# Performance work log

Hardware: AMD Instinct MI355X
Metric: run time of the kernel (lower is better)

The kernel has to match this reference:

```python
import jax, jax.numpy as jnp
import numpy as np

DIM = 1024
NUM_HEADS = 16
WINDOW_SIZE = 512
HEAD_DIM = DIM // NUM_HEADS
SCALE = HEAD_DIM ** (-0.5)


def setup_inputs() -> dict:
    key = jax.random.key(0)
    kq, kk, kv = jax.random.split(key, 3)
    shape = (2, NUM_HEADS, 2048, HEAD_DIM)
    q = jax.random.normal(kq, shape, dtype=jnp.float32)
    k = jax.random.normal(kk, shape, dtype=jnp.float32)
    v = jax.random.normal(kv, shape, dtype=jnp.float32)
    return {"q": q, "k": k, "v": v}


def reference(q, k, v):
    B, H, N, D = q.shape
    pos = jnp.arange(N)
    # causal + sliding window: col <= row and col >= row - w + 1
    window_mask = (pos[None, :] <= pos[:, None]) & (pos[None, :] >= pos[:, None] - WINDOW_SIZE + 1)  # (N, N)
    attn = jnp.einsum("bhnd,bhmd->bhnm", q, k) * SCALE  # (B, H, N, N)
    attn = jnp.where(window_mask[None, None], attn, -jnp.inf)
    attn = jax.nn.softmax(attn, axis=-1)
    attn = jnp.nan_to_num(attn, nan=0.0)
    return jnp.einsum("bhnm,bhmd->bhnd", attn, v)
```

## Files before the change

kernel.cpp:

```cpp
#include <hip/hip_runtime.h>
#include <math.h>


#define SEQ 2048
#define HD  64
#define LDR 72

typedef short short8 __attribute__((ext_vector_type(8)));
typedef float f32x4  __attribute__((ext_vector_type(4)));

static __device__ inline unsigned short f2bf(float f){
  union{float f; unsigned u;} un; un.f=f;
  return (unsigned short)((un.u + 0x7FFFu + ((un.u>>16)&1u))>>16);
}
static __device__ inline int swz(int row){ return (row&3)|(((row>>3)&1)<<2); }

static __device__ __forceinline__ void gll16(const unsigned short* g, unsigned short* l){
  __builtin_amdgcn_global_load_lds(
    (const __attribute__((address_space(1))) unsigned int*)(const void*)g,
    (__attribute__((address_space(3))) unsigned int*)(void*)l, 16, 0, 0);
}

__global__ __launch_bounds__(256) void swa_prep(
    const float* __restrict__ k, const float* __restrict__ v,
    unsigned short* __restrict__ Kb, unsigned short* __restrict__ Vtb)
{
  __shared__ unsigned short Vs[64*68];
  const int tid=threadIdx.x, bid=blockIdx.x;
  const long tbase=(long)bid*4096;
  const float C=0.18033688011112042f;

  #pragma unroll
  for(int i=0;i<2;++i){
    int id=i*256+tid, r=id>>3, lc=id&7;
    float4 f0=*(const float4*)(k+tbase+r*64+lc*8);
    float4 f1=*(const float4*)(k+tbase+r*64+lc*8+4);
    unsigned short h[8];
    h[0]=f2bf(f0.x*C); h[1]=f2bf(f0.y*C); h[2]=f2bf(f0.z*C); h[3]=f2bf(f0.w*C);
    h[4]=f2bf(f1.x*C); h[5]=f2bf(f1.y*C); h[6]=f2bf(f1.z*C); h[7]=f2bf(f1.w*C);
    *(uint4*)(Kb+tbase+r*64+(long)((lc^swz(r))*8))=*(uint4*)h;
  }
  #pragma unroll
  for(int i=0;i<2;++i){
    int id=i*256+tid, r=id>>3, c=id&7;
    float4 f0=*(const float4*)(v+tbase+r*64+c*8);
    float4 f1=*(const float4*)(v+tbase+r*64+c*8+4);
    ushort4 a,b;
    a.x=f2bf(f0.x); a.y=f2bf(f0.y); a.z=f2bf(f0.z); a.w=f2bf(f0.w);
    b.x=f2bf(f1.x); b.y=f2bf(f1.y); b.z=f2bf(f1.z); b.w=f2bf(f1.w);
    *(ushort4*)&Vs[r*68+c*8]  =a;
    *(ushort4*)&Vs[r*68+c*8+4]=b;
  }
  __syncthreads();
  #pragma unroll
  for(int i=0;i<2;++i){
    int id=i*256+tid, d=id>>3, lc=id&7;
    unsigned short t8[8];
    #pragma unroll
    for(int e=0;e<8;++e) t8[e]=Vs[(lc*8+e)*68+d];
    *(uint4*)(Vtb+tbase+d*64+(long)((lc^swz(d))*8))=*(uint4*)t8;
  }
}

__global__ __launch_bounds__(256) void swa_main(
    const float* __restrict__ q,
    const unsigned short* __restrict__ Kb,
    const unsigned short* __restrict__ Vtb,
    float* __restrict__ out)
{
  __shared__ unsigned short Ks[2][4096];
  __shared__ unsigned short Vsh[2][4096];

  const int tid=threadIdx.x, bid=blockIdx.x;
  const int mtile=bid&31, bh=bid>>5, m0=mtile*64;
  const long base=(long)bh*SEQ*HD;
  const int wv=tid>>6, lane=tid&63, quad=lane>>4, l16=lane&15;
  const int qrow=m0+wv*16+l16;

  short8 qa[2];
  {
    const float* qp=q+base+(long)qrow*HD+quad*8;
    #pragma unroll
    for(int kk=0;kk<2;++kk){
      float4 f0=*(const float4*)(qp+kk*32);
      float4 f1=*(const float4*)(qp+kk*32+4);
      short8 a;
      a[0]=(short)f2bf(f0.x); a[1]=(short)f2bf(f0.y);
      a[2]=(short)f2bf(f0.z); a[3]=(short)f2bf(f0.w);
      a[4]=(short)f2bf(f1.x); a[5]=(short)f2bf(f1.y);
      a[6]=(short)f2bf(f1.z); a[7]=(short)f2bf(f1.w);
      qa[kk]=a;
    }
  }

  const int rbase=8*(l16>>2)+(l16&3);
  const int swk=(l16&3)|(((l16>>2)&1)<<2);
  const int swv=(l16&3)|(((l16>>3)&1)<<2);
  int kaoff[2][4], vboff[2][4];
  #pragma unroll
  for(int kk=0;kk<2;++kk){
    #pragma unroll
    for(int nt=0;nt<4;++nt)
      kaoff[kk][nt]=(rbase+(nt&1)*4+(nt>>1)*32)*64+(((quad+4*kk)^swk)*8);
    #pragma unroll
    for(int dt=0;dt<4;++dt)
      vboff[kk][dt]=(dt*16+l16)*64+(((quad+4*kk)^swv)*8);
  }

  const unsigned short* Kt=Kb +(long)bh*32*4096;
  const unsigned short* Vt=Vtb+(long)bh*32*4096;
  const int seg=wv*1024+lane*8;

  f32x4 oacc[4];
  #pragma unroll
  for(int dt=0;dt<4;++dt) oacc[dt]=(f32x4){0.f,0.f,0.f,0.f};
  float lrun=0.f;

  const int tb=mtile, tlo=(mtile>=8)?(mtile-8):0;

  gll16(Kt+(long)tlo*4096+seg,     &Ks[0][seg]);
  gll16(Kt+(long)tlo*4096+seg+512, &Ks[0][seg+512]);
  gll16(Vt+(long)tlo*4096+seg,     &Vsh[0][seg]);
  gll16(Vt+(long)tlo*4096+seg+512, &Vsh[0][seg+512]);
  __syncthreads();

#define STEP(T, BUF, MASKED) {                                                  \
    if ((T)<tb){                                                                \
      const unsigned short* kn=Kt+(long)((T)+1)*4096;                           \
      const unsigned short* vn=Vt+(long)((T)+1)*4096;                           \
      gll16(kn+seg,     &Ks[(BUF)^1][seg]);                                     \
      gll16(kn+seg+512, &Ks[(BUF)^1][seg+512]);                                 \
      gll16(vn+seg,     &Vsh[(BUF)^1][seg]);                                    \
      gll16(vn+seg+512, &Vsh[(BUF)^1][seg+512]);                                \
    }                                                                           \
    f32x4 sacc[4];                                                              \
    _Pragma("unroll") for(int nt=0;nt<4;++nt) sacc[nt]=(f32x4){0.f,0.f,0.f,0.f};\
    _Pragma("unroll") for(int kk=0;kk<2;++kk){                                  \
      _Pragma("unroll") for(int nt=0;nt<4;++nt){                                \
        short8 ka=*(const short8*)&Ks[BUF][kaoff[kk][nt]];                      \
        sacc[nt]=__builtin_amdgcn_mfma_f32_16x16x32_bf16(ka,qa[kk],sacc[nt],0,0,0); \
      }                                                                         \
    }                                                                           \
    short8 vb[4][2];                                                            \
    _Pragma("unroll") for(int dt=0;dt<4;++dt)                                   \
      _Pragma("unroll") for(int kk=0;kk<2;++kk)                                 \
        vb[dt][kk]=*(const short8*)&Vsh[BUF][vboff[kk][dt]];                    \
    unsigned short pb[16];                                                      \
    _Pragma("unroll") for(int nt=0;nt<4;++nt){                                  \
      _Pragma("unroll") for(int r=0;r<4;++r){                                   \
        float e=__builtin_amdgcn_exp2f(sacc[nt][r]);                            \
        if (MASKED){                                                            \
          int key=(T)*64+8*quad+r+(nt&1)*4+(nt>>1)*32;                          \
          bool valid=(key<=qrow)&&(key+511>=qrow);                              \
          e=valid?e:0.f;                                                        \
        }                                                                       \
        lrun+=e;                                                                \
        pb[nt*4+r]=f2bf(e);                                                     \
      }                                                                         \
    }                                                                           \
    short8 pa0,pa1;                                                             \
    _Pragma("unroll") for(int j=0;j<8;++j){ pa0[j]=(short)pb[j]; pa1[j]=(short)pb[8+j]; } \
    _Pragma("unroll") for(int dt=0;dt<4;++dt){                                  \
      oacc[dt]=__builtin_amdgcn_mfma_f32_16x16x32_bf16(pa0,vb[dt][0],oacc[dt],0,0,0); \
      oacc[dt]=__builtin_amdgcn_mfma_f32_16x16x32_bf16(pa1,vb[dt][1],oacc[dt],0,0,0); \
    }                                                                           \
    __syncthreads();                                                            \
  }

  if (mtile>=8){
    STEP(tlo, 0, true);
    for(int t=tlo+1;t<tb;++t) STEP(t, (t-tlo)&1, false);
    STEP(tb, 0, true);
  } else {
    for(int t=0;t<tb;++t) STEP(t, t&1, false);
    STEP(tb, tb&1, true);
  }
#undef STEP

  lrun+=__shfl_xor(lrun,16);
  lrun+=__shfl_xor(lrun,32);
  float linv=1.0f/lrun;
  #pragma unroll
  for(int r=0;r<4;++r){
    float lr=__shfl(linv,quad*4+r);
    const int orow=m0+wv*16+quad*4+r;
    #pragma unroll
    for(int dt=0;dt<4;++dt)
      out[base+(long)orow*HD+dt*16+l16]=oacc[dt][r]*lr;
  }
}

__global__ __launch_bounds__(256) void swa_fwd(
    const float* __restrict__ q, const float* __restrict__ k,
    const float* __restrict__ v, float* __restrict__ out)
{
  __shared__ short Qs[64*LDR];
  __shared__ short Ps[64*LDR];
  __shared__ short Ksh[2][64*LDR];
  __shared__ short Vtr[2][HD*LDR];

  const int tid=threadIdx.x, bid=blockIdx.x;
  const int mtile=bid&31, bh=bid>>5, m0=mtile*64;
  const long base=(long)bh*SEQ*HD;
  const int wv=tid>>6, lane=tid&63, quad=lane>>4, l16=lane&15;
  const int dcol=lane;

  {
    const float4* qg=(const float4*)(q+base+(long)m0*HD);
    #pragma unroll
    for(int i=0;i<4;++i){
      int idx=i*256+tid, r=idx>>4, c4=idx&15;
      float4 f=qg[idx];
      ushort4 h; h.x=f2bf(f.x); h.y=f2bf(f.y); h.z=f2bf(f.z); h.w=f2bf(f.w);
      *(ushort4*)&Qs[r*LDR+c4*4]=h;
    }
  }
  const int tb=mtile, tlo=(tb>8)?(tb-8):0;
  float4 kreg[4]; float vcol[4][4];
  {
    const float4* kg=(const float4*)(k+base+(long)(tlo*64)*HD);
    const float*  vg=v+base+(long)(tlo*64)*HD;
    #pragma unroll
    for(int i=0;i<4;++i) kreg[i]=kg[i*256+tid];
    #pragma unroll
    for(int g=0;g<4;++g){ int r0=wv*4+g*16;
      #pragma unroll
      for(int j=0;j<4;++j) vcol[g][j]=vg[(r0+j)*HD+dcol]; }
  }
  __syncthreads();
  short8 qa[2];
  #pragma unroll
  for(int kk=0;kk<2;++kk)
    qa[kk]=*(const short8*)&Qs[(wv*16+l16)*LDR+kk*32+quad*8];
  {
    #pragma unroll
    for(int i=0;i<4;++i){
      int idx=i*256+tid, r=idx>>4, c4=idx&15;
      float4 fk=kreg[i];
      ushort4 hk; hk.x=f2bf(fk.x); hk.y=f2bf(fk.y); hk.z=f2bf(fk.z); hk.w=f2bf(fk.w);
      *(ushort4*)&Ksh[0][r*LDR+c4*4]=hk;
    }
    #pragma unroll
    for(int g=0;g<4;++g){ int r0=wv*4+g*16;
      ushort4 hv; hv.x=f2bf(vcol[g][0]); hv.y=f2bf(vcol[g][1]);
                  hv.z=f2bf(vcol[g][2]); hv.w=f2bf(vcol[g][3]);
      *(ushort4*)&Vtr[0][dcol*LDR+r0]=hv; }
  }
  float lrun[4]={0.f,0.f,0.f,0.f};
  f32x4 oacc[4];
  #pragma unroll
  for(int dt=0;dt<4;++dt) oacc[dt]=(f32x4){0.f,0.f,0.f,0.f};
  __syncthreads();

  for(int t=tlo;t<=tb;++t){
    const int buf=(t-tlo)&1, j0=t*64;
    f32x4 sacc[4];
    #pragma unroll
    for(int nt=0;nt<4;++nt) sacc[nt]=(f32x4){0.f,0.f,0.f,0.f};
    #pragma unroll
    for(int kk=0;kk<2;++kk){
      #pragma unroll
      for(int nt=0;nt<4;++nt){
        short8 kb=*(const short8*)&Ksh[buf][(nt*16+l16)*LDR+kk*32+quad*8];
        sacc[nt]=__builtin_amdgcn_mfma_f32_16x16x32_bf16(qa[kk],kb,sacc[nt],0,0,0);
      }
    }
    if(t<tb){
      const float4* kg=(const float4*)(k+base+(long)((t+1)*64)*HD);
      const float*  vg=v+base+(long)((t+1)*64)*HD;
      #pragma unroll
      for(int i=0;i<4;++i) kreg[i]=kg[i*256+tid];
      #pragma unroll
      for(int g=0;g<4;++g){ int r0=wv*4+g*16;
        #pragma unroll
        for(int j=0;j<4;++j) vcol[g][j]=vg[(r0+j)*HD+dcol]; }
    }
    #pragma unroll
    for(int r=0;r<4;++r){
      const int grr=m0+wv*16+quad*4+r;
      #pragma unroll
      for(int nt=0;nt<4;++nt){
        const int gc=j0+nt*16+l16;
        float e=exp2f(sacc[nt][r]*0.18033688011112042f);
        float p=((gc<=grr)&&(gc>=grr-511))?e:0.f;
        lrun[r]+=p;
        Ps[(wv*16+quad*4+r)*LDR+nt*16+l16]=(short)f2bf(p);
      }
    }
    __syncthreads();
    #pragma unroll
    for(int kk=0;kk<2;++kk){
      short8 pa=*(const short8*)&Ps[(wv*16+l16)*LDR+kk*32+quad*8];
      #pragma unroll
      for(int dt=0;dt<4;++dt){
        short8 vb=*(const short8*)&Vtr[buf][(dt*16+l16)*LDR+kk*32+quad*8];
        oacc[dt]=__builtin_amdgcn_mfma_f32_16x16x32_bf16(pa,vb,oacc[dt],0,0,0);
      }
    }
    if(t<tb){
      #pragma unroll
      for(int i=0;i<4;++i){
        int idx=i*256+tid, r=idx>>4, c4=idx&15;
        float4 fk=kreg[i];
        ushort4 hk; hk.x=f2bf(fk.x); hk.y=f2bf(fk.y); hk.z=f2bf(fk.z); hk.w=f2bf(fk.w);
        *(ushort4*)&Ksh[buf^1][r*LDR+c4*4]=hk;
      }
      #pragma unroll
      for(int g=0;g<4;++g){ int r0=wv*4+g*16;
        ushort4 hv; hv.x=f2bf(vcol[g][0]); hv.y=f2bf(vcol[g][1]);
                    hv.z=f2bf(vcol[g][2]); hv.w=f2bf(vcol[g][3]);
        *(ushort4*)&Vtr[buf^1][dcol*LDR+r0]=hv; }
    }
    __syncthreads();
  }
  #pragma unroll
  for(int r=0;r<4;++r){
    float s=lrun[r];
    s+=__shfl_xor(s,1); s+=__shfl_xor(s,2); s+=__shfl_xor(s,4); s+=__shfl_xor(s,8);
    lrun[r]=(s>0.f)?(1.f/s):0.f;
  }
  #pragma unroll
  for(int r=0;r<4;++r){
    const int row=m0+wv*16+quad*4+r;
    #pragma unroll
    for(int dt=0;dt<4;++dt)
      out[base+(long)row*HD+dt*16+l16]=oacc[dt][r]*lrun[r];
  }
}

extern "C" void kernel_launch(void* const* d_in, const int* in_sizes, int n_in,
                              void* d_out, int out_size, void* d_ws, size_t ws_size,
                              hipStream_t stream) {
  (void)in_sizes; (void)n_in; (void)out_size;
  const float* q=(const float*)d_in[0];
  const float* k=(const float*)d_in[1];
  const float* v=(const float*)d_in[2];
  float* o=(float*)d_out;
  const size_t NEED = 2ull*32*2048*64*2;
  if (ws_size>=NEED){
    unsigned short* Kb =(unsigned short*)d_ws;
    unsigned short* Vtb=Kb+32ull*2048*64;
    hipLaunchKernelGGL(swa_prep, dim3(1024), dim3(256), 0, stream, k, v, Kb, Vtb);
    hipLaunchKernelGGL(swa_main, dim3(1024), dim3(256), 0, stream, q, Kb, Vtb, o);
  } else {
    hipLaunchKernelGGL(swa_fwd, dim3(1024), dim3(256), 0, stream, q, k, v, o);
  }
}
```

Baseline: 117.2 us.

## Use 128-row query tiles with 8 waves sharing K/V tiles; swizzle prep LDS

The main attention kernel now processes 128 query rows per block with 512 threads, so two 64-row halves share each K/V tile loaded into LDS, which halves redundant global loads of K/V. Each half only computes on the tiles inside its own window, and the loop now picks masked or unmasked softmax at run time. The prep kernel also XOR-swizzles the V staging layout to cut LDS bank conflicts in the transpose. In exchange there are half as many blocks, fewer waves can be resident, and the half-sets idle on edge tiles that only the other half uses.

```diff
diff --git a/kernel.cpp b/kernel.cpp
--- a/kernel.cpp
+++ b/kernel.cpp
@@ -35,21 +35,22 @@
     int id=i*256+tid, r=id>>3, lc=id&7;
     float4 f0=*(const float4*)(k+tbase+r*64+lc*8);
     float4 f1=*(const float4*)(k+tbase+r*64+lc*8+4);
-    unsigned short h[8];
-    h[0]=f2bf(f0.x*C); h[1]=f2bf(f0.y*C); h[2]=f2bf(f0.z*C); h[3]=f2bf(f0.w*C);
-    h[4]=f2bf(f1.x*C); h[5]=f2bf(f1.y*C); h[6]=f2bf(f1.z*C); h[7]=f2bf(f1.w*C);
-    *(uint4*)(Kb+tbase+r*64+(long)((lc^swz(r))*8))=*(uint4*)h;
+    unsigned short hh[8];
+    hh[0]=f2bf(f0.x*C); hh[1]=f2bf(f0.y*C); hh[2]=f2bf(f0.z*C); hh[3]=f2bf(f0.w*C);
+    hh[4]=f2bf(f1.x*C); hh[5]=f2bf(f1.y*C); hh[6]=f2bf(f1.z*C); hh[7]=f2bf(f1.w*C);
+    *(uint4*)(Kb+tbase+r*64+(long)((lc^swz(r))*8))=*(uint4*)hh;
   }
   #pragma unroll
   for(int i=0;i<2;++i){
     int id=i*256+tid, r=id>>3, c=id&7;
+    int phys=(c^(r>>3))&7;
     float4 f0=*(const float4*)(v+tbase+r*64+c*8);
     float4 f1=*(const float4*)(v+tbase+r*64+c*8+4);
     ushort4 a,b;
     a.x=f2bf(f0.x); a.y=f2bf(f0.y); a.z=f2bf(f0.z); a.w=f2bf(f0.w);
     b.x=f2bf(f1.x); b.y=f2bf(f1.y); b.z=f2bf(f1.z); b.w=f2bf(f1.w);
-    *(ushort4*)&Vs[r*68+c*8]  =a;
-    *(ushort4*)&Vs[r*68+c*8+4]=b;
+    *(ushort4*)&Vs[r*68+phys*8]  =a;
+    *(ushort4*)&Vs[r*68+phys*8+4]=b;
   }
   __syncthreads();
   #pragma unroll
@@ -57,12 +58,16 @@
     int id=i*256+tid, d=id>>3, lc=id&7;
     unsigned short t8[8];
     #pragma unroll
-    for(int e=0;e<8;++e) t8[e]=Vs[(lc*8+e)*68+d];
+    for(int e=0;e<8;++e){
+      int key=lc*8+e;
+      int phys=((d>>3)^lc)&7;
+      t8[e]=Vs[key*68 + phys*8 + (d&7)];
+    }
     *(uint4*)(Vtb+tbase+d*64+(long)((lc^swz(d))*8))=*(uint4*)t8;
   }
 }
 
-__global__ __launch_bounds__(256) void swa_main(
+__global__ __launch_bounds__(512) void swa_main(
     const float* __restrict__ q,
     const unsigned short* __restrict__ Kb,
     const unsigned short* __restrict__ Vtb,
@@ -72,10 +77,11 @@
   __shared__ unsigned short Vsh[2][4096];
 
   const int tid=threadIdx.x, bid=blockIdx.x;
-  const int mtile=bid&31, bh=bid>>5, m0=mtile*64;
+  const int mt=bid&15, bh=bid>>4, m0=mt*128;
   const long base=(long)bh*SEQ*HD;
   const int wv=tid>>6, lane=tid&63, quad=lane>>4, l16=lane&15;
   const int qrow=m0+wv*16+l16;
+  const int h=wv>>2;
 
   short8 qa[2];
   {
@@ -109,73 +115,85 @@
 
   const unsigned short* Kt=Kb +(long)bh*32*4096;
   const unsigned short* Vt=Vtb+(long)bh*32*4096;
-  const int seg=wv*1024+lane*8;
+  const int seg=tid*8;
 
   f32x4 oacc[4];
   #pragma unroll
   for(int dt=0;dt<4;++dt) oacc[dt]=(f32x4){0.f,0.f,0.f,0.f};
   float lrun=0.f;
 
-  const int tb=mtile, tlo=(mtile>=8)?(mtile-8):0;
-
-  gll16(Kt+(long)tlo*4096+seg,     &Ks[0][seg]);
-  gll16(Kt+(long)tlo*4096+seg+512, &Ks[0][seg+512]);
-  gll16(Vt+(long)tlo*4096+seg,     &Vsh[0][seg]);
-  gll16(Vt+(long)tlo*4096+seg+512, &Vsh[0][seg+512]);
+  const int Tb  =2*mt+1;
+  const int Tlo =(2*mt>8)?(2*mt-8):0;
+  const int myTb=2*mt+h;
+  const int myTlo=(myTb>=8)?(myTb-8):0;
+  const bool clip=(myTb>=8);
+
+  gll16(Kt+(long)Tlo*4096+seg, &Ks[0][seg]);
+  gll16(Vt+(long)Tlo*4096+seg, &Vsh[0][seg]);
   __syncthreads();
 
-#define STEP(T, BUF, MASKED) {                                                  \
-    if ((T)<tb){                                                                \
-      const unsigned short* kn=Kt+(long)((T)+1)*4096;                           \
-      const unsigned short* vn=Vt+(long)((T)+1)*4096;                           \
-      gll16(kn+seg,     &Ks[(BUF)^1][seg]);                                     \
-      gll16(kn+seg+512, &Ks[(BUF)^1][seg+512]);                                 \
-      gll16(vn+seg,     &Vsh[(BUF)^1][seg]);                                    \
-      gll16(vn+seg+512, &Vsh[(BUF)^1][seg+512]);                                \
-    }                                                                           \
-    f32x4 sacc[4];                                                              \
-    _Pragma("unroll") for(int nt=0;nt<4;++nt) sacc[nt]=(f32x4){0.f,0.f,0.f,0.f};\
-    _Pragma("unroll") for(int kk=0;kk<2;++kk){                                  \
-      _Pragma("unroll") for(int nt=0;nt<4;++nt){                                \
-        short8 ka=*(const short8*)&Ks[BUF][kaoff[kk][nt]];                      \
-        sacc[nt]=__builtin_amdgcn_mfma_f32_16x16x32_bf16(ka,qa[kk],sacc[nt],0,0,0); \
-      }                                                                         \
-    }                                                                           \
-    short8 vb[4][2];                                                            \
-    _Pragma("unroll") for(int dt=0;dt<4;++dt)                                   \
-      _Pragma("unroll") for(int kk=0;kk<2;++kk)                                 \
-        vb[dt][kk]=*(const short8*)&Vsh[BUF][vboff[kk][dt]];                    \
-    unsigned short pb[16];                                                      \
-    _Pragma("unroll") for(int nt=0;nt<4;++nt){                                  \
-      _Pragma("unroll") for(int r=0;r<4;++r){                                   \
-        float e=__builtin_amdgcn_exp2f(sacc[nt][r]);                            \
-        if (MASKED){                                                            \
-          int key=(T)*64+8*quad+r+(nt&1)*4+(nt>>1)*32;                          \
-          bool valid=(key<=qrow)&&(key+511>=qrow);                              \
-          e=valid?e:0.f;                                                        \
-        }                                                                       \
-        lrun+=e;                                                                \
-        pb[nt*4+r]=f2bf(e);                                                     \
-      }                                                                         \
-    }                                                                           \
-    short8 pa0,pa1;                                                             \
-    _Pragma("unroll") for(int j=0;j<8;++j){ pa0[j]=(short)pb[j]; pa1[j]=(short)pb[8+j]; } \
-    _Pragma("unroll") for(int dt=0;dt<4;++dt){                                  \
-      oacc[dt]=__builtin_amdgcn_mfma_f32_16x16x32_bf16(pa0,vb[dt][0],oacc[dt],0,0,0); \
-      oacc[dt]=__builtin_amdgcn_mfma_f32_16x16x32_bf16(pa1,vb[dt][1],oacc[dt],0,0,0); \
-    }                                                                           \
-    __syncthreads();                                                            \
-  }
-
-  if (mtile>=8){
-    STEP(tlo, 0, true);
-    for(int t=tlo+1;t<tb;++t) STEP(t, (t-tlo)&1, false);
-    STEP(tb, 0, true);
-  } else {
-    for(int t=0;t<tb;++t) STEP(t, t&1, false);
-    STEP(tb, tb&1, true);
-  }
-#undef STEP
+  for(int t=Tlo;t<=Tb;++t){
+    const int buf=(t-Tlo)&1;
+    if(t<Tb){
+      gll16(Kt+(long)(t+1)*4096+seg, &Ks[buf^1][seg]);
+      gll16(Vt+(long)(t+1)*4096+seg, &Vsh[buf^1][seg]);
+    }
+    if(t>=myTlo && t<=myTb){
+      f32x4 sacc[4];
+      #pragma unroll
+      for(int nt=0;nt<4;++nt) sacc[nt]=(f32x4){0.f,0.f,0.f,0.f};
+      #pragma unroll
+      for(int kk=0;kk<2;++kk){
+        #pragma unroll
+        for(int nt=0;nt<4;++nt){
+          short8 ka=*(const short8*)&Ks[buf][kaoff[kk][nt]];
+          sacc[nt]=__builtin_amdgcn_mfma_f32_16x16x32_bf16(ka,qa[kk],sacc[nt],0,0,0);
+        }
+      }
+      short8 vb[4][2];
+      #pragma unroll
+      for(int dt=0;dt<4;++dt)
+        #pragma unroll
+        for(int kk=0;kk<2;++kk)
+          vb[dt][kk]=*(const short8*)&Vsh[buf][vboff[kk][dt]];
+
+      unsigned short pb[16];
+      const bool msk=(t==myTb)||(clip&&t==myTlo);
+      if(msk){
+        #pragma unroll
+        for(int nt=0;nt<4;++nt){
+          #pragma unroll
+          for(int r=0;r<4;++r){
+            float e=__builtin_amdgcn_exp2f(sacc[nt][r]);
+            int key=t*64+8*quad+r+(nt&1)*4+(nt>>1)*32;
+            bool valid=(key<=qrow)&&(key+511>=qrow);
+            e=valid?e:0.f;
+            lrun+=e;
+            pb[nt*4+r]=f2bf(e);
+          }
+        }
+      } else {
+        #pragma unroll
+        for(int nt=0;nt<4;++nt){
+          #pragma unroll
+          for(int r=0;r<4;++r){
+            float e=__builtin_amdgcn_exp2f(sacc[nt][r]);
+            lrun+=e;
+            pb[nt*4+r]=f2bf(e);
+          }
+        }
+      }
+      short8 pa0,pa1;
+      #pragma unroll
+      for(int j=0;j<8;++j){ pa0[j]=(short)pb[j]; pa1[j]=(short)pb[8+j]; }
+      #pragma unroll
+      for(int dt=0;dt<4;++dt){
+        oacc[dt]=__builtin_amdgcn_mfma_f32_16x16x32_bf16(pa0,vb[dt][0],oacc[dt],0,0,0);
+        oacc[dt]=__builtin_amdgcn_mfma_f32_16x16x32_bf16(pa1,vb[dt][1],oacc[dt],0,0,0);
+      }
+    }
+    __syncthreads();
+  }
 
   lrun+=__shfl_xor(lrun,16);
   lrun+=__shfl_xor(lrun,32);
@@ -211,8 +229,8 @@
     for(int i=0;i<4;++i){
       int idx=i*256+tid, r=idx>>4, c4=idx&15;
       float4 f=qg[idx];
-      ushort4 h; h.x=f2bf(f.x); h.y=f2bf(f.y); h.z=f2bf(f.z); h.w=f2bf(f.w);
-      *(ushort4*)&Qs[r*LDR+c4*4]=h;
+      ushort4 hh; hh.x=f2bf(f.x); hh.y=f2bf(f.y); hh.z=f2bf(f.z); hh.w=f2bf(f.w);
+      *(ushort4*)&Qs[r*LDR+c4*4]=hh;
     }
   }
   const int tb=mtile, tlo=(tb>8)?(tb-8):0;
@@ -341,7 +359,7 @@
     unsigned short* Kb =(unsigned short*)d_ws;
     unsigned short* Vtb=Kb+32ull*2048*64;
     hipLaunchKernelGGL(swa_prep, dim3(1024), dim3(256), 0, stream, k, v, Kb, Vtb);
-    hipLaunchKernelGGL(swa_main, dim3(1024), dim3(256), 0, stream, q, Kb, Vtb, o);
+    hipLaunchKernelGGL(swa_main, dim3(512),  dim3(512), 0, stream, q, Kb, Vtb, o);
   } else {
     hipLaunchKernelGGL(swa_fwd, dim3(1024), dim3(256), 0, stream, q, k, v, o);
   }
```

Result: faster. 110.0 us (-6.1%).
